# Optimization experiments

Measured on AMD Instinct MI355X. Metric: run time of the kernel, lower is better.

The kernel has to match this reference:

```python
import jax, jax.numpy as jnp
import numpy as np

B, L, ENC, DEC, EMB, ATT, V, T = 64, 49, 2048, 512, 512, 256, 10000, 50

def setup_inputs() -> dict:
    key = jax.random.key(0)
    ks = jax.random.split(key, 20)
    s = 0.02
    return {
        "spatial_feats": jax.random.normal(ks[0], (B, L, ENC), jnp.float32),
        "captions": jax.random.randint(ks[1], (B, T), 0, V),
        # linear_feat: encoder_dim -> decoder_dim
        "W_feat": jax.random.normal(ks[2], (ENC, DEC), jnp.float32) * s,
        "b_feat": jnp.zeros((DEC,), jnp.float32),
        # BahdanauAttention linears
        "W_ea": jax.random.normal(ks[3], (DEC, ATT), jnp.float32) * s,
        "b_ea": jnp.zeros((ATT,), jnp.float32),
        "W_da": jax.random.normal(ks[4], (DEC, ATT), jnp.float32) * s,
        "b_da": jnp.zeros((ATT,), jnp.float32),
        "W_fa": jax.random.normal(ks[5], (ATT, 1), jnp.float32) * s,
        "b_fa": jnp.zeros((1,), jnp.float32),
        # embedding table
        "emb": jax.random.normal(ks[6], (V, EMB), jnp.float32) * s,
        # GRU (torch layout: [3*H, In] / [3*H, H]), input = EMB + DEC
        "W_ih": jax.random.normal(ks[7], (3 * DEC, EMB + DEC), jnp.float32) * s,
        "W_hh": jax.random.normal(ks[8], (3 * DEC, DEC), jnp.float32) * s,
        "b_ih": jnp.zeros((3 * DEC,), jnp.float32),
        "b_hh": jnp.zeros((3 * DEC,), jnp.float32),
        # fc: decoder_dim -> vocab
        "W_fc": jax.random.normal(ks[9], (DEC, V), jnp.float32) * s,
        "b_fc": jnp.zeros((V,), jnp.float32),
    }

def _gru_cell(x, h, W_ih, W_hh, b_ih, b_hh):
    # torch nn.GRU single-step semantics
    gi = x @ W_ih.T + b_ih  # [B, 3H]
    gh = h @ W_hh.T + b_hh
    i_r, i_z, i_n = jnp.split(gi, 3, axis=-1)
    h_r, h_z, h_n = jnp.split(gh, 3, axis=-1)
    r = jax.nn.sigmoid(i_r + h_r)
    z = jax.nn.sigmoid(i_z + h_z)
    n = jnp.tanh(i_n + r * h_n)
    return (1.0 - z) * n + z * h

def reference(spatial_feats, captions, W_feat, b_feat, W_ea, b_ea, W_da, b_da,
              W_fa, b_fa, emb, W_ih, W_hh, b_ih, b_hh, W_fc, b_fc):
    enc = spatial_feats @ W_feat + b_feat            # [B, L, DEC]
    att1 = enc @ W_ea + b_ea                          # [B, L, ATT] (loop-invariant)
    embeddings = emb[captions]                        # [B, T, EMB]
    h0 = jnp.zeros((enc.shape[0], W_hh.shape[1]), enc.dtype)

    def step(h, emb_t):
        # Bahdanau attention
        att2 = h @ W_da + b_da                        # [B, ATT]
        att = (jnp.tanh(att1 + att2[:, None, :]) @ W_fa + b_fa)[..., 0]  # [B, L]
        alpha = jax.nn.softmax(att, axis=1)
        context = jnp.einsum('bl,bld->bd', alpha, enc)
        # single-step GRU + fc
        x = jnp.concatenate([emb_t, context], axis=-1)
        h_new = _gru_cell(x, h, W_ih, W_hh, b_ih, b_hh)
        logits = h_new @ W_fc + b_fc                  # [B, V]
        return h_new, logits

    _, outs = jax.lax.scan(step, h0, jnp.transpose(embeddings, (1, 0, 2)))
    return jnp.transpose(outs, (1, 0, 2))             # [B, T, V]
```

## Files before the change

### kernel.cpp

```cpp
#include <hip/hip_runtime.h>


static __device__ __forceinline__ float my_tanh(float x) {
    x = fminf(fmaxf(x, -15.f), 15.f);
    float e = __expf(2.f * x);
    return (e - 1.f) / (e + 1.f);
}
static __device__ __forceinline__ float my_sigmoid(float x) {
    return 1.f / (1.f + __expf(-x));
}

__global__ __launch_bounds__(256) void transpose_f32(
    const float* __restrict__ in, float* __restrict__ out,
    int R, int C, int ld_in)
{
    __shared__ float tile[32][33];
    int tc = blockIdx.x * 32;
    int tr = blockIdx.y * 32;
    int tx = threadIdx.x & 31, ty = threadIdx.x >> 5;
    #pragma unroll
    for (int i = 0; i < 4; i++) {
        int r = tr + ty + i * 8, c = tc + tx;
        tile[ty + i * 8][tx] = (r < R && c < C) ? in[(long)r * ld_in + c] : 0.f;
    }
    __syncthreads();
    #pragma unroll
    for (int i = 0; i < 4; i++) {
        int c = tc + ty + i * 8, r = tr + tx;
        if (c < C && r < R) out[(long)c * R + r] = tile[tx][ty + i * 8];
    }
}

__global__ __launch_bounds__(256) void gemm_tile_f32(
    const float* __restrict__ A, int lda,
    const float* __restrict__ B, int ldb,
    const float* __restrict__ bias,
    float* __restrict__ C, int ldc,
    int M, int N, int K)
{
    __shared__ float As[16 * 132];
    __shared__ float Bs[16 * 132];
    const int tid = threadIdx.x;
    const int tx = tid & 15, ty = tid >> 4;
    const int rbase = blockIdx.y * 128;
    const int cbase = blockIdx.x * 128;

    float acc8[8][8];
    #pragma unroll
    for (int i = 0; i < 8; ++i)
        #pragma unroll
        for (int j = 0; j < 8; ++j) acc8[i][j] = 0.f;

    for (int kt = 0; kt < K; kt += 16) {
        #pragma unroll
        for (int u = 0; u < 2; ++u) {
            const int f = tid + u * 256;
            const int m = f >> 2, kq = f & 3;
            int row = rbase + m; if (row > M - 1) row = M - 1;
            const float4 v = *(const float4*)(A + (size_t)row * lda + kt + kq * 4);
            As[(kq * 4 + 0) * 132 + m] = v.x;
            As[(kq * 4 + 1) * 132 + m] = v.y;
            As[(kq * 4 + 2) * 132 + m] = v.z;
            As[(kq * 4 + 3) * 132 + m] = v.w;
        }
        #pragma unroll
        for (int u = 0; u < 2; ++u) {
            const int f = tid + u * 256;
            const int krow = f >> 5, nq = f & 31;
            int col = cbase + nq * 4; if (col > N - 4) col = N - 4;
            *(float4*)(&Bs[krow * 132 + nq * 4]) =
                *(const float4*)(B + (size_t)(kt + krow) * ldb + col);
        }
        __syncthreads();
        #pragma unroll
        for (int kk = 0; kk < 16; ++kk) {
            const float4 a0 = *(const float4*)(&As[kk * 132 + ty * 4]);
            const float4 a1 = *(const float4*)(&As[kk * 132 + 64 + ty * 4]);
            const float4 b0 = *(const float4*)(&Bs[kk * 132 + tx * 4]);
            const float4 b1 = *(const float4*)(&Bs[kk * 132 + 64 + tx * 4]);
            const float av[8] = {a0.x,a0.y,a0.z,a0.w,a1.x,a1.y,a1.z,a1.w};
            const float bv[8] = {b0.x,b0.y,b0.z,b0.w,b1.x,b1.y,b1.z,b1.w};
            #pragma unroll
            for (int i = 0; i < 8; ++i)
                #pragma unroll
                for (int j = 0; j < 8; ++j)
                    acc8[i][j] = fmaf(av[i], bv[j], acc8[i][j]);
        }
        __syncthreads();
    }

    float4 b4[2];
    #pragma unroll
    for (int cj = 0; cj < 2; ++cj) {
        const int col = cbase + cj * 64 + tx * 4;
        if (col < N && bias) {
            b4[cj].x = bias[col]; b4[cj].y = bias[col + 1];
            b4[cj].z = bias[col + 2]; b4[cj].w = bias[col + 3];
        } else { b4[cj].x = b4[cj].y = b4[cj].z = b4[cj].w = 0.f; }
    }
    #pragma unroll
    for (int i = 0; i < 8; ++i) {
        const int row = rbase + (i >> 2) * 64 + ty * 4 + (i & 3);
        if (row >= M) continue;
        #pragma unroll
        for (int cj = 0; cj < 2; ++cj) {
            const int col = cbase + cj * 64 + tx * 4;
            if (col >= N) continue;
            float4 o;
            o.x = acc8[i][cj * 4 + 0] + b4[cj].x;
            o.y = acc8[i][cj * 4 + 1] + b4[cj].y;
            o.z = acc8[i][cj * 4 + 2] + b4[cj].z;
            o.w = acc8[i][cj * 4 + 3] + b4[cj].w;
            *(float4*)(C + (size_t)row * ldc + col) = o;
        }
    }
}

__global__ __launch_bounds__(256) void gather_emb(
    const int* __restrict__ caps, const float* __restrict__ emb,
    float* __restrict__ out)
{
    const int m = blockIdx.x;
    const int cap = caps[m];
    const float* src = emb + (size_t)cap * 512;
    float* dst = out + (size_t)m * 512;
    dst[threadIdx.x] = src[threadIdx.x];
    dst[threadIdx.x + 256] = src[threadIdx.x + 256];
}

__global__ __launch_bounds__(512) void step_fused(
    const int t,
    const float* __restrict__ att1,
    const float* __restrict__ W_da,
    const float* __restrict__ b_da,
    const float* __restrict__ W_fa,
    const float* __restrict__ b_fa,
    const float* __restrict__ Wt_hh,
    const float* __restrict__ b_hh,
    const float* __restrict__ Gemb,
    const float* __restrict__ P,
    float* __restrict__ h_g,
    float* __restrict__ Hbuf)
{
    __shared__ float sh_h[512];
    __shared__ float sh_a2p[8 * 256];
    __shared__ float sh_att2[256];
    __shared__ float sh_red[392];
    __shared__ float sh_alpha[64];
    __shared__ float sh_gp[16 * 384];
    __shared__ float sh_gh[384];
    __shared__ float sh_gi[384];

    const int tid = threadIdx.x;
    const int b  = blockIdx.x & 63;
    const int sl = blockIdx.x >> 6;

    sh_h[tid] = (t == 0) ? 0.f : h_g[(size_t)b * 512 + tid];
    __syncthreads();

    {
        const int jq = tid & 63, kq = tid >> 6;
        const float4* w4 = (const float4*)(W_da + (size_t)(kq * 64) * 256 + jq * 4);
        const float* hk = sh_h + kq * 64;
        float4 a = {0.f, 0.f, 0.f, 0.f};
        #pragma unroll 8
        for (int k = 0; k < 64; ++k) {
            const float hv = hk[k];
            const float4 w = w4[(size_t)k * 64];
            a.x = fmaf(hv, w.x, a.x); a.y = fmaf(hv, w.y, a.y);
            a.z = fmaf(hv, w.z, a.z); a.w = fmaf(hv, w.w, a.w);
        }
        *(float4*)&sh_a2p[kq * 256 + jq * 4] = a;
    }
    __syncthreads();
    if (tid < 256) {
        float s = b_da[tid];
        #pragma unroll
        for (int kq = 0; kq < 8; ++kq) s += sh_a2p[kq * 256 + tid];
        sh_att2[tid] = s;
    }
    __syncthreads();

    if (tid < 392) {
        const int l = tid >> 3, ch = tid & 7;
        const float4* a4 =
            (const float4*)(att1 + ((size_t)b * 49 + l) * 256 + ch * 32);
        const float* at2 = sh_att2 + ch * 32;
        const float* wf = W_fa + ch * 32;
        float s = 0.f;
        #pragma unroll
        for (int i = 0; i < 8; ++i) {
            const float4 v = a4[i];
            s += my_tanh(v.x + at2[i * 4 + 0]) * wf[i * 4 + 0];
            s += my_tanh(v.y + at2[i * 4 + 1]) * wf[i * 4 + 1];
            s += my_tanh(v.z + at2[i * 4 + 2]) * wf[i * 4 + 2];
            s += my_tanh(v.w + at2[i * 4 + 3]) * wf[i * 4 + 3];
        }
        sh_red[tid] = s;
    }
    __syncthreads();

    if (tid < 64) {
        float v = -1e30f;
        if (tid < 49) {
            const float* r = sh_red + tid * 8;
            v = r[0] + r[1] + r[2] + r[3] + r[4] + r[5] + r[6] + r[7] + b_fa[0];
        }
        float m = v;
        #pragma unroll
        for (int o = 32; o; o >>= 1) m = fmaxf(m, __shfl_xor(m, o));
        const float e = (tid < 49) ? __expf(v - m) : 0.f;
        float su = e;
        #pragma unroll
        for (int o = 32; o; o >>= 1) su += __shfl_xor(su, o);
        sh_alpha[tid] = e / su;
    }
    __syncthreads();

    {
        const int jq = tid & 31, kq = tid >> 5;
        const int jbase = sl * 128 + jq * 4;
        const float* wrow = Wt_hh + (size_t)(kq * 32) * 1536 + jbase;
        const float* hk = sh_h + kq * 32;
        float4 a0 = {0.f,0.f,0.f,0.f}, a1 = {0.f,0.f,0.f,0.f},
               a2 = {0.f,0.f,0.f,0.f};
        #pragma unroll 8
        for (int k = 0; k < 32; ++k) {
            const float hv = hk[k];
            const float4 w0 = *(const float4*)(wrow + (size_t)k * 1536);
            const float4 w1 = *(const float4*)(wrow + (size_t)k * 1536 + 512);
            const float4 w2 = *(const float4*)(wrow + (size_t)k * 1536 + 1024);
            a0.x = fmaf(hv, w0.x, a0.x); a0.y = fmaf(hv, w0.y, a0.y);
            a0.z = fmaf(hv, w0.z, a0.z); a0.w = fmaf(hv, w0.w, a0.w);
            a1.x = fmaf(hv, w1.x, a1.x); a1.y = fmaf(hv, w1.y, a1.y);
            a1.z = fmaf(hv, w1.z, a1.z); a1.w = fmaf(hv, w1.w, a1.w);
            a2.x = fmaf(hv, w2.x, a2.x); a2.y = fmaf(hv, w2.y, a2.y);
            a2.z = fmaf(hv, w2.z, a2.z); a2.w = fmaf(hv, w2.w, a2.w);
        }
        float* gp = sh_gp + kq * 384;
        *(float4*)(gp + jq * 4)       = a0;
        *(float4*)(gp + 128 + jq * 4) = a1;
        *(float4*)(gp + 256 + jq * 4) = a2;
    }
    __syncthreads();

    if (tid < 384) {
        const int g = tid >> 7, jj = tid & 127;
        const int n = g * 512 + sl * 128 + jj;
        float s = 0.f;
        #pragma unroll
        for (int kq = 0; kq < 16; ++kq) s += sh_gp[kq * 384 + tid];
        sh_gh[tid] = s + b_hh[n];

        float gi = Gemb[((size_t)b * 50 + t) * 1536 + n];
        const float* pp = P + (size_t)b * 49 * 1536 + n;
        #pragma unroll 7
        for (int l = 0; l < 49; ++l)
            gi = fmaf(sh_alpha[l], pp[(size_t)l * 1536], gi);
        sh_gi[tid] = gi;
    }
    __syncthreads();

    if (tid < 128) {
        const int j = sl * 128 + tid;
        const float r  = my_sigmoid(sh_gi[tid] + sh_gh[tid]);
        const float z  = my_sigmoid(sh_gi[128 + tid] + sh_gh[128 + tid]);
        const float nn = my_tanh(sh_gi[256 + tid] + r * sh_gh[256 + tid]);
        const float hnew = (1.f - z) * nn + z * sh_h[j];
        h_g[(size_t)b * 512 + j] = hnew;
        Hbuf[((size_t)b * 50 + t) * 512 + j] = hnew;
    }
}

extern "C" void kernel_launch(void* const* d_in, const int* in_sizes, int n_in,
                              void* d_out, int out_size, void* d_ws, size_t ws_size,
                              hipStream_t stream) {
    const float* spatial = (const float*)d_in[0];
    const int*   captions= (const int*)d_in[1];
    const float* W_feat  = (const float*)d_in[2];
    const float* b_feat  = (const float*)d_in[3];
    const float* W_ea    = (const float*)d_in[4];
    const float* b_ea    = (const float*)d_in[5];
    const float* W_da    = (const float*)d_in[6];
    const float* b_da    = (const float*)d_in[7];
    const float* W_fa    = (const float*)d_in[8];
    const float* b_fa    = (const float*)d_in[9];
    const float* emb     = (const float*)d_in[10];
    const float* W_ih    = (const float*)d_in[11];
    const float* W_hh    = (const float*)d_in[12];
    const float* b_ih    = (const float*)d_in[13];
    const float* b_hh    = (const float*)d_in[14];
    const float* W_fc    = (const float*)d_in[15];
    const float* b_fc    = (const float*)d_in[16];
    float* out = (float*)d_out;

    char* ws = (char*)d_ws;
    float* Wt_ih = (float*)ws; ws += (size_t)1024 * 1536 * 4;
    float* Wt_hh = (float*)ws; ws += (size_t)512 * 1536 * 4;
    float* enc   = (float*)ws; ws += (size_t)3136 * 512 * 4;
    float* att1  = (float*)ws; ws += (size_t)3136 * 256 * 4;
    float* Hbuf  = (float*)ws; ws += (size_t)3200 * 512 * 4;
    float* h_g   = (float*)ws; ws += (size_t)64 * 512 * 4;
    const size_t NEED = 6291456ull + 3145728 + 6422528 + 3211264
                      + 6553600 + 131072;
    if (ws_size < NEED) return;

    float* Gemb = out;
    float* P    = out + (size_t)3200 * 1536;
    float* Embt = Hbuf;

    dim3 blk(256);
    transpose_f32<<<dim3(32, 48), blk, 0, stream>>>(W_ih, Wt_ih, 1536, 1024, 1024);
    transpose_f32<<<dim3(16, 48), blk, 0, stream>>>(W_hh, Wt_hh, 1536, 512, 512);

    gather_emb<<<dim3(3200), blk, 0, stream>>>(captions, emb, Embt);

    gemm_tile_f32<<<dim3(4, 25), blk, 0, stream>>>(spatial, 2048, W_feat, 512,
                                                   b_feat, enc, 512,
                                                   3136, 512, 2048);
    gemm_tile_f32<<<dim3(2, 25), blk, 0, stream>>>(enc, 512, W_ea, 256, b_ea,
                                                   att1, 256, 3136, 256, 512);
    gemm_tile_f32<<<dim3(12, 25), blk, 0, stream>>>(Embt, 512, Wt_ih, 1536, b_ih,
                                                    Gemb, 1536, 3200, 1536, 512);
    gemm_tile_f32<<<dim3(12, 25), blk, 0, stream>>>(
        enc, 512, Wt_ih + (size_t)512 * 1536, 1536, (const float*)nullptr,
        P, 1536, 3136, 1536, 512);

    for (int t = 0; t < 50; ++t)
        step_fused<<<dim3(256), dim3(512), 0, stream>>>(
            t, att1, W_da, b_da, W_fa, b_fa, Wt_hh, b_hh, Gemb, P, h_g, Hbuf);

    gemm_tile_f32<<<dim3(79, 25), blk, 0, stream>>>(Hbuf, 512, W_fc, 10000, b_fc,
                                                    out, 10000, 3200, 10000, 512);
}
```

Measured before the change: 2.250 ms.

## Prefetch P slice into shared memory early and reorder step phases

The per-step kernel now issues the global loads of its 49x384 P slice and Gemb value at kernel start, holds them in registers and stages them to shared memory after the W_hh matvec. The attention chain (att2 reduce, tanh scores, softmax) moves after the W_hh matvec, with the att2 reduction done by the idle threads alongside the gh reduction. The aim is to overlap P's global-memory latency with the matvecs and drop one barrier. In exchange the kernel uses about 75KB more shared memory and 40 extra registers per thread, which may cut occupancy or cause spills.

```diff
diff --git a/kernel.cpp b/kernel.cpp
--- a/kernel.cpp
+++ b/kernel.cpp
@@ -143,6 +143,7 @@
     float* __restrict__ Hbuf)
 {
     __shared__ float sh_h[512];
+    __shared__ float sh_P[49 * 384];
     __shared__ float sh_a2p[8 * 256];
     __shared__ float sh_att2[256];
     __shared__ float sh_red[392];
@@ -156,8 +157,26 @@
     const int sl = blockIdx.x >> 6;
 
     sh_h[tid] = (t == 0) ? 0.f : h_g[(size_t)b * 512 + tid];
-    __syncthreads();
-
+    float gemb_reg = 0.f;
+    if (tid < 384) {
+        const int n = (tid >> 7) * 512 + sl * 128 + (tid & 127);
+        gemb_reg = Gemb[((size_t)b * 50 + t) * 1536 + n];
+    }
+    __syncthreads();
+
+    float4 pr[10];
+    {
+        const float* Pb = P + (size_t)b * 49 * 1536 + sl * 128;
+        #pragma unroll
+        for (int u = 0; u < 10; ++u) {
+            const int i = tid + u * 512;
+            if (i < 4704) {
+                const int l = i / 96, r = i - l * 96;
+                const int g = r >> 5, jj = r & 31;
+                pr[u] = *(const float4*)(Pb + (size_t)l * 1536 + g * 512 + jj * 4);
+            }
+        }
+    }
     {
         const int jq = tid & 63, kq = tid >> 6;
         const float4* w4 = (const float4*)(W_da + (size_t)(kq * 64) * 256 + jq * 4);
@@ -172,51 +191,6 @@
         }
         *(float4*)&sh_a2p[kq * 256 + jq * 4] = a;
     }
-    __syncthreads();
-    if (tid < 256) {
-        float s = b_da[tid];
-        #pragma unroll
-        for (int kq = 0; kq < 8; ++kq) s += sh_a2p[kq * 256 + tid];
-        sh_att2[tid] = s;
-    }
-    __syncthreads();
-
-    if (tid < 392) {
-        const int l = tid >> 3, ch = tid & 7;
-        const float4* a4 =
-            (const float4*)(att1 + ((size_t)b * 49 + l) * 256 + ch * 32);
-        const float* at2 = sh_att2 + ch * 32;
-        const float* wf = W_fa + ch * 32;
-        float s = 0.f;
-        #pragma unroll
-        for (int i = 0; i < 8; ++i) {
-            const float4 v = a4[i];
-            s += my_tanh(v.x + at2[i * 4 + 0]) * wf[i * 4 + 0];
-            s += my_tanh(v.y + at2[i * 4 + 1]) * wf[i * 4 + 1];
-            s += my_tanh(v.z + at2[i * 4 + 2]) * wf[i * 4 + 2];
-            s += my_tanh(v.w + at2[i * 4 + 3]) * wf[i * 4 + 3];
-        }
-        sh_red[tid] = s;
-    }
-    __syncthreads();
-
-    if (tid < 64) {
-        float v = -1e30f;
-        if (tid < 49) {
-            const float* r = sh_red + tid * 8;
-            v = r[0] + r[1] + r[2] + r[3] + r[4] + r[5] + r[6] + r[7] + b_fa[0];
-        }
-        float m = v;
-        #pragma unroll
-        for (int o = 32; o; o >>= 1) m = fmaxf(m, __shfl_xor(m, o));
-        const float e = (tid < 49) ? __expf(v - m) : 0.f;
-        float su = e;
-        #pragma unroll
-        for (int o = 32; o; o >>= 1) su += __shfl_xor(su, o);
-        sh_alpha[tid] = e / su;
-    }
-    __syncthreads();
-
     {
         const int jq = tid & 31, kq = tid >> 5;
         const int jbase = sl * 128 + jq * 4;
@@ -242,6 +216,16 @@
         *(float4*)(gp + 128 + jq * 4) = a1;
         *(float4*)(gp + 256 + jq * 4) = a2;
     }
+    {
+        #pragma unroll
+        for (int u = 0; u < 10; ++u) {
+            const int i = tid + u * 512;
+            if (i < 4704) {
+                const int l = i / 96, r = i - l * 96;
+                *(float4*)&sh_P[l * 384 + r * 4] = pr[u];
+            }
+        }
+    }
     __syncthreads();
 
     if (tid < 384) {
@@ -251,12 +235,61 @@
         #pragma unroll
         for (int kq = 0; kq < 16; ++kq) s += sh_gp[kq * 384 + tid];
         sh_gh[tid] = s + b_hh[n];
-
-        float gi = Gemb[((size_t)b * 50 + t) * 1536 + n];
-        const float* pp = P + (size_t)b * 49 * 1536 + n;
+    } else {
+        const int j0 = (tid - 384) * 2;
+        #pragma unroll
+        for (int u = 0; u < 2; ++u) {
+            const int j = j0 + u;
+            float s = b_da[j];
+            #pragma unroll
+            for (int kq = 0; kq < 8; ++kq) s += sh_a2p[kq * 256 + j];
+            sh_att2[j] = s;
+        }
+    }
+    __syncthreads();
+
+    if (tid < 392) {
+        const int l = tid >> 3, ch = tid & 7;
+        const float4* a4 =
+            (const float4*)(att1 + ((size_t)b * 49 + l) * 256 + ch * 32);
+        const float* at2 = sh_att2 + ch * 32;
+        const float* wf = W_fa + ch * 32;
+        float s = 0.f;
+        #pragma unroll
+        for (int i = 0; i < 8; ++i) {
+            const float4 v = a4[i];
+            s += my_tanh(v.x + at2[i * 4 + 0]) * wf[i * 4 + 0];
+            s += my_tanh(v.y + at2[i * 4 + 1]) * wf[i * 4 + 1];
+            s += my_tanh(v.z + at2[i * 4 + 2]) * wf[i * 4 + 2];
+            s += my_tanh(v.w + at2[i * 4 + 3]) * wf[i * 4 + 3];
+        }
+        sh_red[tid] = s;
+    }
+    __syncthreads();
+
+    if (tid < 64) {
+        float v = -1e30f;
+        if (tid < 49) {
+            const float* r = sh_red + tid * 8;
+            v = r[0] + r[1] + r[2] + r[3] + r[4] + r[5] + r[6] + r[7] + b_fa[0];
+        }
+        float m = v;
+        #pragma unroll
+        for (int o = 32; o; o >>= 1) m = fmaxf(m, __shfl_xor(m, o));
+        const float e = (tid < 49) ? __expf(v - m) : 0.f;
+        float su = e;
+        #pragma unroll
+        for (int o = 32; o; o >>= 1) su += __shfl_xor(su, o);
+        sh_alpha[tid] = e / su;
+    }
+    __syncthreads();
+
+    if (tid < 384) {
+        float gi = gemb_reg;
+        const float* pp = sh_P + tid;
         #pragma unroll 7
         for (int l = 0; l < 49; ++l)
-            gi = fmaf(sh_alpha[l], pp[(size_t)l * 1536], gi);
+            gi = fmaf(sh_alpha[l], pp[l * 384], gi);
         sh_gi[tid] = gi;
     }
     __syncthreads();
```

New measurement: 2.329 ms. 1.04x slower.

## Split recurrent step into score and gate kernels, batch four rows per gate block

Applied to the files above, without the earlier changes.

The per-timestep fused kernel is split in two. A score kernel computes attention scores split across four column chunks per batch row. A gate kernel then processes four batch rows per block over a 32-column slice, so each W_hh weight is reused across four hidden states, and it stages the P slice in shared memory while the recurrent matvec runs. This removes the redundant per-row attention work and cuts W_hh traffic. The cost is twice as many launches per step, plus large shared memory per block (about 80KB) that may limit occupancy.

```diff
diff --git a/kernel.cpp b/kernel.cpp
--- a/kernel.cpp
+++ b/kernel.cpp
@@ -128,12 +128,78 @@
     dst[threadIdx.x + 256] = src[threadIdx.x + 256];
 }
 
-__global__ __launch_bounds__(512) void step_fused(
+__global__ __launch_bounds__(256) void score_step(
     const int t,
     const float* __restrict__ att1,
     const float* __restrict__ W_da,
     const float* __restrict__ b_da,
     const float* __restrict__ W_fa,
+    const float* __restrict__ h_g,
+    float* __restrict__ score_part)
+{
+    __shared__ float sh_h[512];
+    __shared__ float sh_a2p[16 * 64];
+    __shared__ float sh_att2[64];
+    __shared__ float sh_sp[196];
+
+    const int tid = threadIdx.x;
+    const int b  = blockIdx.x >> 2;
+    const int jc = blockIdx.x & 3;
+
+    sh_h[tid]       = (t == 0) ? 0.f : h_g[(size_t)b * 512 + tid];
+    sh_h[256 + tid] = (t == 0) ? 0.f : h_g[(size_t)b * 512 + 256 + tid];
+    __syncthreads();
+
+    {
+        const int jq = tid & 15, kq = tid >> 4;
+        const float4* w4 =
+            (const float4*)(W_da + (size_t)(kq * 32) * 256 + jc * 64 + jq * 4);
+        const float* hk = sh_h + kq * 32;
+        float4 a = {0.f, 0.f, 0.f, 0.f};
+        #pragma unroll 8
+        for (int k = 0; k < 32; ++k) {
+            const float hv = hk[k];
+            const float4 w = w4[(size_t)k * 64];
+            a.x = fmaf(hv, w.x, a.x); a.y = fmaf(hv, w.y, a.y);
+            a.z = fmaf(hv, w.z, a.z); a.w = fmaf(hv, w.w, a.w);
+        }
+        *(float4*)&sh_a2p[kq * 64 + jq * 4] = a;
+    }
+    __syncthreads();
+    if (tid < 64) {
+        float s = b_da[jc * 64 + tid];
+        #pragma unroll
+        for (int kq = 0; kq < 16; ++kq) s += sh_a2p[kq * 64 + tid];
+        sh_att2[tid] = s;
+    }
+    __syncthreads();
+    if (tid < 196) {
+        const int l = tid >> 2, q = tid & 3;
+        const float4* a4 =
+            (const float4*)(att1 + ((size_t)b * 49 + l) * 256 + jc * 64 + q * 16);
+        const float* at2 = sh_att2 + q * 16;
+        const float* wf  = W_fa + jc * 64 + q * 16;
+        float s = 0.f;
+        #pragma unroll
+        for (int i = 0; i < 4; ++i) {
+            const float4 v = a4[i];
+            s += my_tanh(v.x + at2[i * 4 + 0]) * wf[i * 4 + 0];
+            s += my_tanh(v.y + at2[i * 4 + 1]) * wf[i * 4 + 1];
+            s += my_tanh(v.z + at2[i * 4 + 2]) * wf[i * 4 + 2];
+            s += my_tanh(v.w + at2[i * 4 + 3]) * wf[i * 4 + 3];
+        }
+        sh_sp[tid] = s;
+    }
+    __syncthreads();
+    if (tid < 49) {
+        const float* r = sh_sp + tid * 4;
+        score_part[((size_t)b * 4 + jc) * 64 + tid] = r[0] + r[1] + r[2] + r[3];
+    }
+}
+
+__global__ __launch_bounds__(512) void gate_step(
+    const int t,
+    const float* __restrict__ score_part,
     const float* __restrict__ b_fa,
     const float* __restrict__ Wt_hh,
     const float* __restrict__ b_hh,
@@ -142,74 +208,35 @@
     float* __restrict__ h_g,
     float* __restrict__ Hbuf)
 {
-    __shared__ float sh_h[512];
-    __shared__ float sh_a2p[8 * 256];
-    __shared__ float sh_att2[256];
-    __shared__ float sh_red[392];
-    __shared__ float sh_alpha[64];
-    __shared__ float sh_gp[16 * 384];
-    __shared__ float sh_gh[384];
-    __shared__ float sh_gi[384];
+    __shared__ float sh_h[4 * 512];
+    __shared__ float sh_alpha[4 * 64];
+    __shared__ float sh_P[4 * 49 * 96];
+    __shared__ float sh_gp[4 * 4 * 96];
+    __shared__ float sh_gh[4 * 96];
+    __shared__ float sh_gi[4 * 96];
 
     const int tid = threadIdx.x;
-    const int b  = blockIdx.x & 63;
-    const int sl = blockIdx.x >> 6;
-
-    sh_h[tid] = (t == 0) ? 0.f : h_g[(size_t)b * 512 + tid];
-    __syncthreads();
-
-    {
-        const int jq = tid & 63, kq = tid >> 6;
-        const float4* w4 = (const float4*)(W_da + (size_t)(kq * 64) * 256 + jq * 4);
-        const float* hk = sh_h + kq * 64;
-        float4 a = {0.f, 0.f, 0.f, 0.f};
-        #pragma unroll 8
-        for (int k = 0; k < 64; ++k) {
-            const float hv = hk[k];
-            const float4 w = w4[(size_t)k * 64];
-            a.x = fmaf(hv, w.x, a.x); a.y = fmaf(hv, w.y, a.y);
-            a.z = fmaf(hv, w.z, a.z); a.w = fmaf(hv, w.w, a.w);
-        }
-        *(float4*)&sh_a2p[kq * 256 + jq * 4] = a;
-    }
-    __syncthreads();
+    const int quad = blockIdx.x >> 4;
+    const int sl   = blockIdx.x & 15;
+    const int b0 = quad * 4;
+
+    for (int i = tid; i < 2048; i += 512)
+        sh_h[i] = (t == 0) ? 0.f : h_g[(size_t)b0 * 512 + i];
+    float gemb_reg = 0.f;
+    if (tid < 384) {
+        const int bb = tid / 96, cc = tid - bb * 96;
+        const int n = (cc >> 5) * 512 + sl * 32 + (cc & 31);
+        gemb_reg = Gemb[((size_t)(b0 + bb) * 50 + t) * 1536 + n];
+    }
     if (tid < 256) {
-        float s = b_da[tid];
-        #pragma unroll
-        for (int kq = 0; kq < 8; ++kq) s += sh_a2p[kq * 256 + tid];
-        sh_att2[tid] = s;
-    }
-    __syncthreads();
-
-    if (tid < 392) {
-        const int l = tid >> 3, ch = tid & 7;
-        const float4* a4 =
-            (const float4*)(att1 + ((size_t)b * 49 + l) * 256 + ch * 32);
-        const float* at2 = sh_att2 + ch * 32;
-        const float* wf = W_fa + ch * 32;
-        float s = 0.f;
-        #pragma unroll
-        for (int i = 0; i < 8; ++i) {
-            const float4 v = a4[i];
-            s += my_tanh(v.x + at2[i * 4 + 0]) * wf[i * 4 + 0];
-            s += my_tanh(v.y + at2[i * 4 + 1]) * wf[i * 4 + 1];
-            s += my_tanh(v.z + at2[i * 4 + 2]) * wf[i * 4 + 2];
-            s += my_tanh(v.w + at2[i * 4 + 3]) * wf[i * 4 + 3];
-        }
-        sh_red[tid] = s;
-    }
-    __syncthreads();
-
-    if (tid < 64) {
+        const int bb = tid >> 6, l = tid & 63;
+        const float* sp = score_part + (size_t)(b0 + bb) * 256;
         float v = -1e30f;
-        if (tid < 49) {
-            const float* r = sh_red + tid * 8;
-            v = r[0] + r[1] + r[2] + r[3] + r[4] + r[5] + r[6] + r[7] + b_fa[0];
-        }
+        if (l < 49) v = sp[l] + sp[64 + l] + sp[128 + l] + sp[192 + l] + b_fa[0];
         float m = v;
         #pragma unroll
         for (int o = 32; o; o >>= 1) m = fmaxf(m, __shfl_xor(m, o));
-        const float e = (tid < 49) ? __expf(v - m) : 0.f;
+        const float e = (l < 49) ? __expf(v - m) : 0.f;
         float su = e;
         #pragma unroll
         for (int o = 32; o; o >>= 1) su += __shfl_xor(su, o);
@@ -217,58 +244,64 @@
     }
     __syncthreads();
 
-    {
-        const int jq = tid & 31, kq = tid >> 5;
-        const int jbase = sl * 128 + jq * 4;
-        const float* wrow = Wt_hh + (size_t)(kq * 32) * 1536 + jbase;
-        const float* hk = sh_h + kq * 32;
-        float4 a0 = {0.f,0.f,0.f,0.f}, a1 = {0.f,0.f,0.f,0.f},
-               a2 = {0.f,0.f,0.f,0.f};
+    if (tid < 384) {
+        const int cc = tid % 96, kq = tid / 96;
+        const int n = (cc >> 5) * 512 + sl * 32 + (cc & 31);
+        const float* wcol = Wt_hh + (size_t)(kq * 128) * 1536 + n;
+        const float* h0 = sh_h + kq * 128;
+        float a0 = 0.f, a1 = 0.f, a2 = 0.f, a3 = 0.f;
         #pragma unroll 8
-        for (int k = 0; k < 32; ++k) {
-            const float hv = hk[k];
-            const float4 w0 = *(const float4*)(wrow + (size_t)k * 1536);
-            const float4 w1 = *(const float4*)(wrow + (size_t)k * 1536 + 512);
-            const float4 w2 = *(const float4*)(wrow + (size_t)k * 1536 + 1024);
-            a0.x = fmaf(hv, w0.x, a0.x); a0.y = fmaf(hv, w0.y, a0.y);
-            a0.z = fmaf(hv, w0.z, a0.z); a0.w = fmaf(hv, w0.w, a0.w);
-            a1.x = fmaf(hv, w1.x, a1.x); a1.y = fmaf(hv, w1.y, a1.y);
-            a1.z = fmaf(hv, w1.z, a1.z); a1.w = fmaf(hv, w1.w, a1.w);
-            a2.x = fmaf(hv, w2.x, a2.x); a2.y = fmaf(hv, w2.y, a2.y);
-            a2.z = fmaf(hv, w2.z, a2.z); a2.w = fmaf(hv, w2.w, a2.w);
-        }
-        float* gp = sh_gp + kq * 384;
-        *(float4*)(gp + jq * 4)       = a0;
-        *(float4*)(gp + 128 + jq * 4) = a1;
-        *(float4*)(gp + 256 + jq * 4) = a2;
+        for (int k = 0; k < 128; ++k) {
+            const float w = wcol[(size_t)k * 1536];
+            a0 = fmaf(h0[k],        w, a0);
+            a1 = fmaf(h0[512 + k],  w, a1);
+            a2 = fmaf(h0[1024 + k], w, a2);
+            a3 = fmaf(h0[1536 + k], w, a3);
+        }
+        sh_gp[(kq * 4 + 0) * 96 + cc] = a0;
+        sh_gp[(kq * 4 + 1) * 96 + cc] = a1;
+        sh_gp[(kq * 4 + 2) * 96 + cc] = a2;
+        sh_gp[(kq * 4 + 3) * 96 + cc] = a3;
+    } else {
+        const int pt = tid - 384;
+        const float* Pb = P + (size_t)b0 * 49 * 1536 + sl * 32;
+        for (int i = pt; i < 4704; i += 128) {
+            const int row = i / 24, cg = i - row * 24;
+            const int g = cg >> 3, j4 = cg & 7;
+            *(float4*)&sh_P[row * 96 + cg * 4] =
+                *(const float4*)(Pb + (size_t)row * 1536 + g * 512 + j4 * 4);
+        }
     }
     __syncthreads();
 
     if (tid < 384) {
-        const int g = tid >> 7, jj = tid & 127;
-        const int n = g * 512 + sl * 128 + jj;
-        float s = 0.f;
-        #pragma unroll
-        for (int kq = 0; kq < 16; ++kq) s += sh_gp[kq * 384 + tid];
-        sh_gh[tid] = s + b_hh[n];
-
-        float gi = Gemb[((size_t)b * 50 + t) * 1536 + n];
-        const float* pp = P + (size_t)b * 49 * 1536 + n;
+        const int bb = tid / 96, cc = tid - bb * 96;
+        const int n = (cc >> 5) * 512 + sl * 32 + (cc & 31);
+        float s = sh_gp[(0 * 4 + bb) * 96 + cc] + sh_gp[(1 * 4 + bb) * 96 + cc]
+                + sh_gp[(2 * 4 + bb) * 96 + cc] + sh_gp[(3 * 4 + bb) * 96 + cc];
+        sh_gh[bb * 96 + cc] = s + b_hh[n];
+
+        float gi = gemb_reg;
+        const float* pp = sh_P + (size_t)bb * 49 * 96 + cc;
+        const float* al = sh_alpha + bb * 64;
         #pragma unroll 7
         for (int l = 0; l < 49; ++l)
-            gi = fmaf(sh_alpha[l], pp[(size_t)l * 1536], gi);
-        sh_gi[tid] = gi;
+            gi = fmaf(al[l], pp[l * 96], gi);
+        sh_gi[bb * 96 + cc] = gi;
     }
     __syncthreads();
 
     if (tid < 128) {
-        const int j = sl * 128 + tid;
-        const float r  = my_sigmoid(sh_gi[tid] + sh_gh[tid]);
-        const float z  = my_sigmoid(sh_gi[128 + tid] + sh_gh[128 + tid]);
-        const float nn = my_tanh(sh_gi[256 + tid] + r * sh_gh[256 + tid]);
-        const float hnew = (1.f - z) * nn + z * sh_h[j];
-        h_g[(size_t)b * 512 + j] = hnew;
-        Hbuf[((size_t)b * 50 + t) * 512 + j] = hnew;
+        const int bb = tid >> 5, jj = tid & 31;
+        const int j = sl * 32 + jj;
+        const float* gh = sh_gh + bb * 96;
+        const float* gi = sh_gi + bb * 96;
+        const float r  = my_sigmoid(gi[jj] + gh[jj]);
+        const float z  = my_sigmoid(gi[32 + jj] + gh[32 + jj]);
+        const float nn = my_tanh(gi[64 + jj] + r * gh[64 + jj]);
+        const float hnew = (1.f - z) * nn + z * sh_h[bb * 512 + j];
+        h_g[(size_t)(b0 + bb) * 512 + j] = hnew;
+        Hbuf[((size_t)(b0 + bb) * 50 + t) * 512 + j] = hnew;
     }
 }
 
@@ -301,8 +334,9 @@
     float* att1  = (float*)ws; ws += (size_t)3136 * 256 * 4;
     float* Hbuf  = (float*)ws; ws += (size_t)3200 * 512 * 4;
     float* h_g   = (float*)ws; ws += (size_t)64 * 512 * 4;
+    float* score = (float*)ws; ws += (size_t)64 * 4 * 64 * 4;
     const size_t NEED = 6291456ull + 3145728 + 6422528 + 3211264
-                      + 6553600 + 131072;
+                      + 6553600 + 131072 + 65536;
     if (ws_size < NEED) return;
 
     float* Gemb = out;
@@ -326,9 +360,12 @@
         enc, 512, Wt_ih + (size_t)512 * 1536, 1536, (const float*)nullptr,
         P, 1536, 3136, 1536, 512);
 
-    for (int t = 0; t < 50; ++t)
-        step_fused<<<dim3(256), dim3(512), 0, stream>>>(
-            t, att1, W_da, b_da, W_fa, b_fa, Wt_hh, b_hh, Gemb, P, h_g, Hbuf);
+    for (int t = 0; t < 50; ++t) {
+        score_step<<<dim3(256), dim3(256), 0, stream>>>(
+            t, att1, W_da, b_da, W_fa, h_g, score);
+        gate_step<<<dim3(256), dim3(512), 0, stream>>>(
+            t, score, b_fa, Wt_hh, b_hh, Gemb, P, h_g, Hbuf);
+    }
 
     gemm_tile_f32<<<dim3(79, 25), blk, 0, stream>>>(Hbuf, 512, W_fc, 10000, b_fc,
                                                     out, 10000, 3200, 10000, 512);
```

After: 2.000 ms. 11.1% less time.
